# Performance work log

Hardware: AMD Instinct MI355X
Metric: run time of the kernel (lower is better)

The kernel has to match this reference:

```python
import jax, jax.numpy as jnp
import numpy as np

B, F, V, D, K = 16384, 39, 30000, 16, 20
EPS = 1e-5


def bn_eval(x, g, b):
    # inference-mode BatchNorm1d with running_mean=0, running_var=1
    return g * x / jnp.sqrt(1.0 + EPS) + b


def setup_inputs() -> dict:
    key = jax.random.key(0)
    ks = jax.random.split(key, 12)
    x = jax.random.randint(ks[0], (B, F), 0, V)
    emb_table = jax.random.normal(ks[1], (F * V, D), dtype=jnp.float32) * 0.05
    w_c = jax.random.normal(ks[2], (F, F * D), dtype=jnp.float32) * 0.05
    w0 = jax.random.normal(ks[3], (1024, F * D), dtype=jnp.float32) * 0.04
    w1 = jax.random.normal(ks[4], (512, 1024), dtype=jnp.float32) * 0.03
    w_out = jax.random.normal(ks[5], (1, 512), dtype=jnp.float32) * 0.04
    return {
        'x': x, 'emb_table': emb_table,
        'w_c': w_c, 'b_c': jnp.zeros((F,)), 'g_c': jnp.ones((F,)), 'be_c': jnp.zeros((F,)),
        'w0': w0, 'b0': jnp.zeros((1024,)), 'g0': jnp.ones((1024,)), 'be0': jnp.zeros((1024,)),
        'w1': w1, 'b1': jnp.zeros((512,)), 'g1': jnp.ones((512,)), 'be1': jnp.zeros((512,)),
        'w_out': w_out, 'b_out': jnp.zeros((1,)),
    }


def reference(x, emb_table, w_c, b_c, g_c, be_c, w0, b0, g0, be0,
              w1, b1, g1, be1, w_out, b_out):
    offsets = jnp.arange(F, dtype=x.dtype) * V          # per-field offsets
    idx = x + offsets[None, :]                          # [B, F]
    emb = emb_table[idx]                                # [B, F, D] gather

    # controller_mlp: flatten (batch, D, F) layout like torch transpose(1,2)
    flat = jnp.transpose(emb, (0, 2, 1)).reshape(B, F * D)
    h = jax.nn.relu(bn_eval(flat @ w_c.T + b_c, g_c, be_c))
    scores = jax.nn.softmax(h, axis=1)                  # [B, F]

    # kmax_pooling: top-k field indices, sorted ascending, gather weights
    _, kidx = jax.lax.top_k(scores, K)
    kidx = jnp.sort(kidx, axis=1)                       # [B, K]
    w = jnp.take_along_axis(scores, kidx, axis=1)       # [B, K]

    # forward_select: gather selected field embeddings, weight them
    sel = jnp.take_along_axis(emb, kidx[:, :, None], axis=1)  # [B, K, D]
    weighted = sel * w[:, :, None]

    # scatter back into full field slots (unselected fields are zero)
    full = jnp.zeros((B, F, D), weighted.dtype)
    bidx = jnp.arange(B)[:, None]
    full = full.at[bidx, kidx].set(weighted)            # [B, F, D]

    z = jnp.transpose(full, (0, 2, 1)).reshape(B, F * D)
    z = jax.nn.relu(bn_eval(z @ w0.T + b0, g0, be0))
    z = jax.nn.relu(bn_eval(z @ w1.T + b1, g1, be1))
    out = jax.nn.sigmoid(z @ w_out.T + b_out)           # [B, 1]
    return out.squeeze(-1)
```

## Files before the change

kernel.cpp:

```cpp
#include <hip/hip_runtime.h>
#include <math.h>

#define B_SZ 16384
#define F_N 39
#define V_N 30000
#define D_N 16
#define K_SEL 20
#define FD 624
#define KP0 640
#define NCP 48
#define N0 1024
#define N1 512
#define CBR 16
#define ALD 648

typedef unsigned short u16;
typedef __attribute__((ext_vector_type(8))) short bf16x8;
typedef __attribute__((ext_vector_type(8))) unsigned short u16x8;
typedef __attribute__((ext_vector_type(4))) float f32x4;
typedef __attribute__((ext_vector_type(4))) unsigned short u16x4;

__device__ __forceinline__ u16 f2bf(float v) {
    union { float f; unsigned u; } x; x.f = v;
    unsigned r = x.u + 0x7fff + ((x.u >> 16) & 1);
    return (u16)(r >> 16);
}
__device__ __forceinline__ float bf2f(u16 v) {
    union { unsigned u; float f; } x; x.u = ((unsigned)v) << 16;
    return x.f;
}

#define GLD16(gp, lp) __builtin_amdgcn_global_load_lds( \
    (const __attribute__((address_space(1))) unsigned int*)(gp), \
    (__attribute__((address_space(3))) unsigned int*)(lp), 16, 0, 0)

__global__ void convert_kernel(const float* __restrict__ src, u16* __restrict__ dst,
                               int n_el)
{
    int i = blockIdx.x * blockDim.x + threadIdx.x;
    if (i < n_el) dst[i] = f2bf(src[i]);
}

__global__ void prep_w0_kernel(const float* __restrict__ w0, u16* __restrict__ w0p)
{
    int i = blockIdx.x * blockDim.x + threadIdx.x;
    if (i >= N0 * KP0) return;
    int n = i / KP0, kk = i - n * KP0;
    float v = 0.f;
    if (kk < FD) {
        int f = kk >> 4, d = kk & 15;
        v = w0[n * FD + d * F_N + f];
    }
    w0p[i] = f2bf(v);
}

__global__ void prep_wc_kernel(const float* __restrict__ w_c, u16* __restrict__ wcb)
{
    int i = blockIdx.x * blockDim.x + threadIdx.x;
    if (i >= NCP * KP0) return;
    int n = i / KP0, kk = i - n * KP0;
    float v = 0.f;
    if (n < F_N && kk < FD) {
        int f = kk >> 4, d = kk & 15;
        v = w_c[n * FD + d * F_N + f];
    }
    wcb[i] = f2bf(v);
}

__global__ void pad_params_kernel(const float* __restrict__ b_c,
                                  const float* __restrict__ g_c,
                                  const float* __restrict__ be_c,
                                  float* __restrict__ bp, float* __restrict__ gp,
                                  float* __restrict__ bep)
{
    int n = threadIdx.x;
    bp[n]  = (n < F_N) ? b_c[n]  : 0.f;
    gp[n]  = (n < F_N) ? g_c[n]  : 0.f;
    bep[n] = (n < F_N) ? be_c[n] : 0.f;
}

__global__ __launch_bounds__(256) void fused_controller_kernel(
    const int* __restrict__ x, const float* __restrict__ emb_table,
    const u16* __restrict__ wcb, const float* __restrict__ bcp,
    const float* __restrict__ gcp, const float* __restrict__ becp,
    u16* __restrict__ zb)
{
    __shared__ __align__(16) u16 Al[CBR * ALD];
    __shared__ float vv[CBR][49];
    __shared__ f32x4 part[4][64][3];
    __shared__ float selw[CBR][F_N];

    const int t    = threadIdx.x;
    const int wave = t >> 6;
    const int lane = t & 63;
    const int b0   = blockIdx.x * CBR;

    for (int p = t; p < CBR * F_N; p += 256) {
        const int row = p / F_N;
        const int f   = p - row * F_N;
        const int xi  = x[b0 * F_N + p];
        const float4* src = (const float4*)(emb_table + (size_t)(xi + f * V_N) * D_N);
        float4 v0 = src[0], v1 = src[1], v2 = src[2], v3 = src[3];
        u16x8 o0 = { f2bf(v0.x), f2bf(v0.y), f2bf(v0.z), f2bf(v0.w),
                     f2bf(v1.x), f2bf(v1.y), f2bf(v1.z), f2bf(v1.w) };
        u16x8 o1 = { f2bf(v2.x), f2bf(v2.y), f2bf(v2.z), f2bf(v2.w),
                     f2bf(v3.x), f2bf(v3.y), f2bf(v3.z), f2bf(v3.w) };
        *(u16x8*)&Al[row * ALD + f * D_N]     = o0;
        *(u16x8*)&Al[row * ALD + f * D_N + 8] = o1;
    }
    __syncthreads();

    const int m = lane & 15;
    const int q = lane >> 4;
    f32x4 acc0 = {}, acc1 = {}, acc2 = {};
    {
        const u16* ap  = &Al[m * ALD + wave * 160 + q * 8];
        const u16* bp0 = wcb + (size_t)(0  + m) * KP0 + wave * 160 + q * 8;
        const u16* bp1 = wcb + (size_t)(16 + m) * KP0 + wave * 160 + q * 8;
        const u16* bp2 = wcb + (size_t)(32 + m) * KP0 + wave * 160 + q * 8;
        #pragma unroll
        for (int k = 0; k < 5; ++k) {
            bf16x8 af = *(const bf16x8*)ap;
            bf16x8 b0 = *(const bf16x8*)bp0;
            bf16x8 b1 = *(const bf16x8*)bp1;
            bf16x8 b2 = *(const bf16x8*)bp2;
            acc0 = __builtin_amdgcn_mfma_f32_16x16x32_bf16(af, b0, acc0, 0, 0, 0);
            acc1 = __builtin_amdgcn_mfma_f32_16x16x32_bf16(af, b1, acc1, 0, 0, 0);
            acc2 = __builtin_amdgcn_mfma_f32_16x16x32_bf16(af, b2, acc2, 0, 0, 0);
            ap += 32; bp0 += 32; bp1 += 32; bp2 += 32;
        }
    }
    part[wave][lane][0] = acc0;
    part[wave][lane][1] = acc1;
    part[wave][lane][2] = acc2;
    __syncthreads();

    if (wave == 0) {
        f32x4 r0 = part[0][lane][0] + part[1][lane][0] + part[2][lane][0] + part[3][lane][0];
        f32x4 r1 = part[0][lane][1] + part[1][lane][1] + part[2][lane][1] + part[3][lane][1];
        f32x4 r2 = part[0][lane][2] + part[1][lane][2] + part[2][lane][2] + part[3][lane][2];

        const float rs = rsqrtf(1.0f + 1e-5f);
        #pragma unroll
        for (int j = 0; j < 3; ++j) {
            const f32x4 a = (j == 0) ? r0 : (j == 1) ? r1 : r2;
            const int n = j * 16 + m;
            const float gn = gcp[n] * rs;
            const float bn = becp[n];
            const float bi = bcp[n];
            #pragma unroll
            for (int r = 0; r < 4; ++r)
                vv[q * 4 + r][n] = fmaxf(fmaf(gn, a[r] + bi, bn), 0.f);
        }

        const int row = lane >> 2;
        const int fg  = lane & 3;
        float e[10];
        float mloc = -1e30f;
        #pragma unroll
        for (int it = 0; it < 10; ++it) {
            const int f = fg + 4 * it;
            if (f < F_N) { e[it] = vv[row][f]; mloc = fmaxf(mloc, e[it]); }
        }
        mloc = fmaxf(mloc, __shfl_xor(mloc, 1, 64));
        mloc = fmaxf(mloc, __shfl_xor(mloc, 2, 64));
        float sloc = 0.f;
        #pragma unroll
        for (int it = 0; it < 10; ++it) {
            const int f = fg + 4 * it;
            if (f < F_N) { e[it] = expf(e[it] - mloc); sloc += e[it]; }
        }
        sloc += __shfl_xor(sloc, 1, 64);
        sloc += __shfl_xor(sloc, 2, 64);
        const float inv = 1.f / sloc;
        #pragma unroll
        for (int it = 0; it < 10; ++it) {
            const int f = fg + 4 * it;
            if (f < F_N) vv[row][f] = e[it];
        }

        int rank[10] = {};
        for (int gg = 0; gg < F_N; ++gg) {
            const float o = vv[row][gg];
            #pragma unroll
            for (int it = 0; it < 10; ++it) {
                const int f = fg + 4 * it;
                if (f < F_N)
                    rank[it] += (o > e[it] || (o == e[it] && gg < f)) ? 1 : 0;
            }
        }
        #pragma unroll
        for (int it = 0; it < 10; ++it) {
            const int f = fg + 4 * it;
            if (f < F_N)
                selw[row][f] = (rank[it] < K_SEL) ? e[it] * inv : 0.f;
        }
    }
    __syncthreads();

    for (int gp = t; gp < CBR * 40; gp += 256) {
        const int row  = gp & 15;
        const int slot = gp >> 4;
        u16* dst = zb + (size_t)(b0 + row) * KP0 + slot * D_N;
        u16x8 o0 = {0,0,0,0,0,0,0,0}, o1 = {0,0,0,0,0,0,0,0};
        if (slot < F_N) {
            const float w = selw[row][slot];
            u16x8 a0 = *(u16x8*)&Al[row * ALD + slot * D_N];
            u16x8 a1 = *(u16x8*)&Al[row * ALD + slot * D_N + 8];
            #pragma unroll
            for (int k = 0; k < 8; ++k) {
                o0[k] = f2bf(bf2f(a0[k]) * w);
                o1[k] = f2bf(bf2f(a1[k]) * w);
            }
        }
        *(u16x8*)dst = o0;
        *(u16x8*)(dst + 8) = o1;
    }
}

template<int STORE_BF16>
__global__ __launch_bounds__(256) void gemm_mfma_bn_relu(
    const u16* __restrict__ A, const u16* __restrict__ W,
    const float* __restrict__ bias, const float* __restrict__ g,
    const float* __restrict__ be, void* __restrict__ Cout,
    int M, int N, int Kp)
{
    __shared__ __align__(16) u16 As[128 * 32];
    __shared__ __align__(16) u16 Bs[128 * 32];

    const int t    = threadIdx.x;
    const int wave = t >> 6;
    const int lane = t & 63;
    const int wm   = wave >> 1, wn = wave & 1;
    const int m0   = blockIdx.x * 128;
    const int n0   = blockIdx.y * 128;

    const int lr    = lane >> 2;
    const int swz_u = (lane & 3) ^ ((lane >> 3) & 3);
    const u16* gA0 = A + (size_t)(m0 + wave * 32 + lr) * Kp + swz_u * 8;
    const u16* gA1 = gA0 + 16 * (size_t)Kp;
    const u16* gB0 = W + (size_t)(n0 + wave * 32 + lr) * Kp + swz_u * 8;
    const u16* gB1 = gB0 + 16 * (size_t)Kp;
    u16* lA0 = &As[(wave * 32)      * 32];
    u16* lA1 = &As[(wave * 32 + 16) * 32];
    u16* lB0 = &Bs[(wave * 32)      * 32];
    u16* lB1 = &Bs[(wave * 32 + 16) * 32];

    const int q    = lane >> 4;
    const int lr16 = lane & 15;

    int aoff[4], boff[4];
    #pragma unroll
    for (int i = 0; i < 4; ++i) {
        int ra = wm * 64 + i * 16 + lr16;
        aoff[i] = ra * 32 + ((q ^ ((ra >> 1) & 3)) * 8);
        int rb = wn * 64 + i * 16 + lr16;
        boff[i] = rb * 32 + ((q ^ ((rb >> 1) & 3)) * 8);
    }

    f32x4 acc[4][4] = {};

    for (int k0 = 0; k0 < Kp; k0 += 32) {
        GLD16(gA0, lA0); GLD16(gA1, lA1);
        GLD16(gB0, lB0); GLD16(gB1, lB1);
        gA0 += 32; gA1 += 32; gB0 += 32; gB1 += 32;
        __syncthreads();

        bf16x8 af[4], bfr[4];
        #pragma unroll
        for (int i = 0; i < 4; ++i) af[i]  = *(const bf16x8*)&As[aoff[i]];
        #pragma unroll
        for (int j = 0; j < 4; ++j) bfr[j] = *(const bf16x8*)&Bs[boff[j]];

        #pragma unroll
        for (int i = 0; i < 4; ++i)
            #pragma unroll
            for (int j = 0; j < 4; ++j)
                acc[i][j] = __builtin_amdgcn_mfma_f32_16x16x32_bf16(
                    bfr[j], af[i], acc[i][j], 0, 0, 0);
        __syncthreads();
    }

    const float rs = rsqrtf(1.0f + 1e-5f);
    #pragma unroll
    for (int j = 0; j < 4; ++j) {
        const int nb = n0 + wn * 64 + j * 16 + q * 4;
        const float4 bi4 = *(const float4*)&bias[nb];
        const float4 g4  = *(const float4*)&g[nb];
        const float4 be4 = *(const float4*)&be[nb];
        #pragma unroll
        for (int i = 0; i < 4; ++i) {
            const int m = m0 + wm * 64 + i * 16 + lr16;
            u16x4 ob;
            float4 of;
            #pragma unroll
            for (int r = 0; r < 4; ++r) {
                float v = acc[i][j][r] + (&bi4.x)[r];
                v = fmaxf(fmaf((&g4.x)[r] * rs, v, (&be4.x)[r]), 0.f);
                if (STORE_BF16) ob[r] = f2bf(v);
                else            (&of.x)[r] = v;
            }
            if (STORE_BF16)
                *(u16x4*)((u16*)Cout + (size_t)m * N + nb) = ob;
            else
                *(float4*)((float*)Cout + (size_t)m * N + nb) = of;
        }
    }
}

__global__ __launch_bounds__(256) void out_kernel(
    const u16* __restrict__ h1b, const float* __restrict__ w_out,
    const float* __restrict__ b_out, float* __restrict__ out)
{
    const int wave = threadIdx.x >> 6;
    const int lane = threadIdx.x & 63;
    const int b = blockIdx.x * 4 + wave;
    const u16* row = h1b + (size_t)b * N1;
    float s = 0.f;
    #pragma unroll
    for (int i = 0; i < 8; ++i) {
        int k = lane + i * 64;
        s = fmaf(bf2f(row[k]), w_out[k], s);
    }
    #pragma unroll
    for (int off = 32; off; off >>= 1) s += __shfl_down(s, off, 64);
    if (lane == 0) out[b] = 1.f / (1.f + expf(-(s + b_out[0])));
}

extern "C" void kernel_launch(void* const* d_in, const int* in_sizes, int n_in,
                              void* d_out, int out_size, void* d_ws, size_t ws_size,
                              hipStream_t stream)
{
    const int*   x     = (const int*)  d_in[0];
    const float* emb   = (const float*)d_in[1];
    const float* w_c   = (const float*)d_in[2];
    const float* b_c   = (const float*)d_in[3];
    const float* g_c   = (const float*)d_in[4];
    const float* be_c  = (const float*)d_in[5];
    const float* w0    = (const float*)d_in[6];
    const float* b0    = (const float*)d_in[7];
    const float* g0    = (const float*)d_in[8];
    const float* be0   = (const float*)d_in[9];
    const float* w1    = (const float*)d_in[10];
    const float* b1    = (const float*)d_in[11];
    const float* g1    = (const float*)d_in[12];
    const float* be1   = (const float*)d_in[13];
    const float* w_out = (const float*)d_in[14];
    const float* b_out = (const float*)d_in[15];
    float* out = (float*)d_out;

    u16*   zb    = (u16*)d_ws;
    u16*   w0b   = zb    + (size_t)B_SZ * KP0;
    u16*   h0b   = w0b   + (size_t)N0 * KP0;
    u16*   w1b   = h0b   + (size_t)B_SZ * N0;
    u16*   h1b   = w1b   + (size_t)N1 * N0;
    u16*   wcb   = h1b   + (size_t)B_SZ * N1;
    float* bcp   = (float*)(wcb + (size_t)NCP * KP0);
    float* gcp   = bcp + NCP;
    float* becp  = gcp + NCP;

    pad_params_kernel<<<1, NCP, 0, stream>>>(b_c, g_c, be_c, bcp, gcp, becp);
    prep_wc_kernel<<<(NCP * KP0 + 255) / 256, 256, 0, stream>>>(w_c, wcb);
    prep_w0_kernel<<<(N0 * KP0 + 255) / 256, 256, 0, stream>>>(w0, w0b);
    convert_kernel<<<(N1 * N0 + 255) / 256, 256, 0, stream>>>(w1, w1b, N1 * N0);

    fused_controller_kernel<<<B_SZ / CBR, 256, 0, stream>>>(
        x, emb, wcb, bcp, gcp, becp, zb);

    gemm_mfma_bn_relu<1><<<dim3(B_SZ / 128, N0 / 128), 256, 0, stream>>>(
        zb, w0b, b0, g0, be0, h0b, B_SZ, N0, KP0);
    gemm_mfma_bn_relu<1><<<dim3(B_SZ / 128, N1 / 128), 256, 0, stream>>>(
        h0b, w1b, b1, g1, be1, h1b, B_SZ, N1, N0);

    out_kernel<<<B_SZ / 4, 256, 0, stream>>>(h1b, w_out, b_out, out);
}
```

Before: 245.9 us.

## Fuse output layer into second GEMM epilogue and merge prep kernels

Merges the four weight/parameter prep kernels into one launch. It swaps the MFMA operand order so each lane holds a column n with four consecutive rows. The second GEMM epilogue then computes the w_out dot product directly via shuffle reductions and atomicAdd into a per-row partial buffer, which removes the h1 store and the separate out_kernel read. A memset and a small sigmoid kernel are added. The first GEMM's epilogue now writes scalar, strided bf16 stores instead of vectorized 4-wide stores, which may hurt h0 write efficiency.

New measurement: 230.7 us. 6.2% less time.

```diff
diff --git a/kernel.cpp b/kernel.cpp
--- a/kernel.cpp
+++ b/kernel.cpp
@@ -34,49 +34,43 @@
     (const __attribute__((address_space(1))) unsigned int*)(gp), \
     (__attribute__((address_space(3))) unsigned int*)(lp), 16, 0, 0)
 
-__global__ void convert_kernel(const float* __restrict__ src, u16* __restrict__ dst,
-                               int n_el)
+#define PREP_W0 (N0 * KP0)
+#define PREP_W1 (N1 * N0)
+#define PREP_WC (NCP * KP0)
+#define PREP_TOT (PREP_W0 + PREP_W1 + PREP_WC + 3 * NCP)
+
+__global__ __launch_bounds__(256) void prep_all_kernel(
+    const float* __restrict__ w0, const float* __restrict__ w1,
+    const float* __restrict__ w_c, const float* __restrict__ b_c,
+    const float* __restrict__ g_c, const float* __restrict__ be_c,
+    u16* __restrict__ w0b, u16* __restrict__ w1b, u16* __restrict__ wcb,
+    float* __restrict__ bcp, float* __restrict__ gcp, float* __restrict__ becp)
 {
     int i = blockIdx.x * blockDim.x + threadIdx.x;
-    if (i < n_el) dst[i] = f2bf(src[i]);
-}
-
-__global__ void prep_w0_kernel(const float* __restrict__ w0, u16* __restrict__ w0p)
-{
-    int i = blockIdx.x * blockDim.x + threadIdx.x;
-    if (i >= N0 * KP0) return;
-    int n = i / KP0, kk = i - n * KP0;
-    float v = 0.f;
-    if (kk < FD) {
-        int f = kk >> 4, d = kk & 15;
-        v = w0[n * FD + d * F_N + f];
-    }
-    w0p[i] = f2bf(v);
-}
-
-__global__ void prep_wc_kernel(const float* __restrict__ w_c, u16* __restrict__ wcb)
-{
-    int i = blockIdx.x * blockDim.x + threadIdx.x;
-    if (i >= NCP * KP0) return;
-    int n = i / KP0, kk = i - n * KP0;
-    float v = 0.f;
-    if (n < F_N && kk < FD) {
-        int f = kk >> 4, d = kk & 15;
-        v = w_c[n * FD + d * F_N + f];
-    }
-    wcb[i] = f2bf(v);
-}
-
-__global__ void pad_params_kernel(const float* __restrict__ b_c,
-                                  const float* __restrict__ g_c,
-                                  const float* __restrict__ be_c,
-                                  float* __restrict__ bp, float* __restrict__ gp,
-                                  float* __restrict__ bep)
-{
-    int n = threadIdx.x;
-    bp[n]  = (n < F_N) ? b_c[n]  : 0.f;
-    gp[n]  = (n < F_N) ? g_c[n]  : 0.f;
-    bep[n] = (n < F_N) ? be_c[n] : 0.f;
+    if (i < PREP_W0) {
+        int n = i / KP0, kk = i - n * KP0;
+        float v = 0.f;
+        if (kk < FD) v = w0[n * FD + (kk & 15) * F_N + (kk >> 4)];
+        w0b[i] = f2bf(v);
+        return;
+    }
+    i -= PREP_W0;
+    if (i < PREP_W1) { w1b[i] = f2bf(w1[i]); return; }
+    i -= PREP_W1;
+    if (i < PREP_WC) {
+        int n = i / KP0, kk = i - n * KP0;
+        float v = 0.f;
+        if (n < F_N && kk < FD) v = w_c[n * FD + (kk & 15) * F_N + (kk >> 4)];
+        wcb[i] = f2bf(v);
+        return;
+    }
+    i -= PREP_WC;
+    if (i < 3 * NCP) {
+        int which = i / NCP, n = i - which * NCP;
+        float v = 0.f;
+        if (n < F_N) v = (which == 0) ? b_c[n] : (which == 1) ? g_c[n] : be_c[n];
+        ((which == 0) ? bcp : (which == 1) ? gcp : becp)[n] = v;
+    }
 }
 
 __global__ __launch_bounds__(256) void fused_controller_kernel(
@@ -218,12 +212,13 @@
     }
 }
 
-template<int STORE_BF16>
+template<int MODE>
 __global__ __launch_bounds__(256) void gemm_mfma_bn_relu(
     const u16* __restrict__ A, const u16* __restrict__ W,
     const float* __restrict__ bias, const float* __restrict__ g,
-    const float* __restrict__ be, void* __restrict__ Cout,
-    int M, int N, int Kp)
+    const float* __restrict__ be, u16* __restrict__ Cout,
+    int M, int N, int Kp,
+    const float* __restrict__ w_out, float* __restrict__ outp)
 {
     __shared__ __align__(16) u16 As[128 * 32];
     __shared__ __align__(16) u16 Bs[128 * 32];
@@ -277,54 +272,76 @@
             #pragma unroll
             for (int j = 0; j < 4; ++j)
                 acc[i][j] = __builtin_amdgcn_mfma_f32_16x16x32_bf16(
-                    bfr[j], af[i], acc[i][j], 0, 0, 0);
+                    af[i], bfr[j], acc[i][j], 0, 0, 0);
         __syncthreads();
     }
 
     const float rs = rsqrtf(1.0f + 1e-5f);
-    #pragma unroll
-    for (int j = 0; j < 4; ++j) {
-        const int nb = n0 + wn * 64 + j * 16 + q * 4;
-        const float4 bi4 = *(const float4*)&bias[nb];
-        const float4 g4  = *(const float4*)&g[nb];
-        const float4 be4 = *(const float4*)&be[nb];
-        #pragma unroll
-        for (int i = 0; i < 4; ++i) {
-            const int m = m0 + wm * 64 + i * 16 + lr16;
-            u16x4 ob;
-            float4 of;
+    if (MODE == 0) {
+        #pragma unroll
+        for (int j = 0; j < 4; ++j) {
+            const int n = n0 + wn * 64 + j * 16 + lr16;
+            const float bn_g = g[n] * rs;
+            const float bn_b = be[n];
+            const float bi   = bias[n];
+            #pragma unroll
+            for (int i = 0; i < 4; ++i) {
+                const int mbase = m0 + wm * 64 + i * 16 + q * 4;
+                #pragma unroll
+                for (int r = 0; r < 4; ++r) {
+                    float v = acc[i][j][r] + bi;
+                    v = fmaxf(fmaf(bn_g, v, bn_b), 0.f);
+                    Cout[(size_t)(mbase + r) * N + n] = f2bf(v);
+                }
+            }
+        }
+    } else {
+        float s[4][4] = {};
+        #pragma unroll
+        for (int j = 0; j < 4; ++j) {
+            const int n = n0 + wn * 64 + j * 16 + lr16;
+            const float bn_g = g[n] * rs;
+            const float bn_b = be[n];
+            const float bi   = bias[n];
+            const float wo   = w_out[n];
+            #pragma unroll
+            for (int i = 0; i < 4; ++i)
+                #pragma unroll
+                for (int r = 0; r < 4; ++r) {
+                    float v = acc[i][j][r] + bi;
+                    v = fmaxf(fmaf(bn_g, v, bn_b), 0.f);
+                    s[i][r] = fmaf(v, wo, s[i][r]);
+                }
+        }
+        #pragma unroll
+        for (int i = 0; i < 4; ++i)
             #pragma unroll
             for (int r = 0; r < 4; ++r) {
-                float v = acc[i][j][r] + (&bi4.x)[r];
-                v = fmaxf(fmaf((&g4.x)[r] * rs, v, (&be4.x)[r]), 0.f);
-                if (STORE_BF16) ob[r] = f2bf(v);
-                else            (&of.x)[r] = v;
-            }
-            if (STORE_BF16)
-                *(u16x4*)((u16*)Cout + (size_t)m * N + nb) = ob;
-            else
-                *(float4*)((float*)Cout + (size_t)m * N + nb) = of;
-        }
-    }
-}
-
-__global__ __launch_bounds__(256) void out_kernel(
-    const u16* __restrict__ h1b, const float* __restrict__ w_out,
-    const float* __restrict__ b_out, float* __restrict__ out)
-{
-    const int wave = threadIdx.x >> 6;
-    const int lane = threadIdx.x & 63;
-    const int b = blockIdx.x * 4 + wave;
-    const u16* row = h1b + (size_t)b * N1;
-    float s = 0.f;
-    #pragma unroll
-    for (int i = 0; i < 8; ++i) {
-        int k = lane + i * 64;
-        s = fmaf(bf2f(row[k]), w_out[k], s);
-    }
-    #pragma unroll
-    for (int off = 32; off; off >>= 1) s += __shfl_down(s, off, 64);
-    if (lane == 0) out[b] = 1.f / (1.f + expf(-(s + b_out[0])));
+                float v = s[i][r];
+                v += __shfl_xor(v, 1, 64);
+                v += __shfl_xor(v, 2, 64);
+                v += __shfl_xor(v, 4, 64);
+                v += __shfl_xor(v, 8, 64);
+                s[i][r] = v;
+            }
+        if (lr16 == 0) {
+            #pragma unroll
+            for (int i = 0; i < 4; ++i) {
+                const int mbase = m0 + wm * 64 + i * 16 + q * 4;
+                #pragma unroll
+                for (int r = 0; r < 4; ++r)
+                    atomicAdd(&outp[mbase + r], s[i][r]);
+            }
+        }
+    }
+}
+
+__global__ __launch_bounds__(256) void sigmoid_kernel(
+    const float* __restrict__ outp, const float* __restrict__ b_out,
+    float* __restrict__ out)
+{
+    const int b = blockIdx.x * 256 + threadIdx.x;
+    out[b] = 1.f / (1.f + expf(-(outp[b] + b_out[0])));
 }
 
 extern "C" void kernel_launch(void* const* d_in, const int* in_sizes, int n_in,
@@ -353,24 +370,25 @@
     u16*   w0b   = zb    + (size_t)B_SZ * KP0;
     u16*   h0b   = w0b   + (size_t)N0 * KP0;
     u16*   w1b   = h0b   + (size_t)B_SZ * N0;
-    u16*   h1b   = w1b   + (size_t)N1 * N0;
-    u16*   wcb   = h1b   + (size_t)B_SZ * N1;
-    float* bcp   = (float*)(wcb + (size_t)NCP * KP0);
+    u16*   wcb   = w1b   + (size_t)N1 * N0;
+    float* outp  = (float*)(wcb + (size_t)NCP * KP0);
+    float* bcp   = outp + B_SZ;
     float* gcp   = bcp + NCP;
     float* becp  = gcp + NCP;
 
-    pad_params_kernel<<<1, NCP, 0, stream>>>(b_c, g_c, be_c, bcp, gcp, becp);
-    prep_wc_kernel<<<(NCP * KP0 + 255) / 256, 256, 0, stream>>>(w_c, wcb);
-    prep_w0_kernel<<<(N0 * KP0 + 255) / 256, 256, 0, stream>>>(w0, w0b);
-    convert_kernel<<<(N1 * N0 + 255) / 256, 256, 0, stream>>>(w1, w1b, N1 * N0);
+    prep_all_kernel<<<(PREP_TOT + 255) / 256, 256, 0, stream>>>(
+        w0, w1, w_c, b_c, g_c, be_c, w0b, w1b, wcb, bcp, gcp, becp);
 
     fused_controller_kernel<<<B_SZ / CBR, 256, 0, stream>>>(
         x, emb, wcb, bcp, gcp, becp, zb);
 
-    gemm_mfma_bn_relu<1><<<dim3(B_SZ / 128, N0 / 128), 256, 0, stream>>>(
-        zb, w0b, b0, g0, be0, h0b, B_SZ, N0, KP0);
+    gemm_mfma_bn_relu<0><<<dim3(B_SZ / 128, N0 / 128), 256, 0, stream>>>(
+        zb, w0b, b0, g0, be0, h0b, B_SZ, N0, KP0, nullptr, nullptr);
+
+    hipMemsetAsync(outp, 0, B_SZ * sizeof(float), stream);
+
     gemm_mfma_bn_relu<1><<<dim3(B_SZ / 128, N1 / 128), 256, 0, stream>>>(
-        h0b, w1b, b1, g1, be1, h1b, B_SZ, N1, N0);
-
-    out_kernel<<<B_SZ / 4, 256, 0, stream>>>(h1b, w_out, b_out, out);
-}
+        h0b, w1b, b1, g1, be1, nullptr, B_SZ, N1, N0, w_out, outp);
+
+    sigmoid_kernel<<<B_SZ / 256, 256, 0, stream>>>(outp, b_out, out);
+}
```
